# Kernel optimization log

Measured on AMD Instinct MI355X. Metric: run time of the kernel, lower is better.

## Reference

```python
import jax, jax.numpy as jnp
import numpy as np

HEADS = 20
NUM_AOE = 16
NUM_IP = 16


def setup_inputs() -> dict:
    key = jax.random.key(0)
    ks = jax.random.split(key, 7)
    B, Sq, H = 8, 4096, 1280
    Skv, C = 109, 768
    scale = 0.02
    return {
        "hidden_states": jax.random.normal(ks[0], (B, Sq, H), jnp.float32),
        "encoder_hidden_states": jax.random.normal(ks[1], (B, Skv, C), jnp.float32),
        "Wq": jax.random.normal(ks[2], (H, H), jnp.float32) * scale,
        "Wk": jax.random.normal(ks[3], (C, H), jnp.float32) * scale,
        "Wv": jax.random.normal(ks[4], (C, H), jnp.float32) * scale,
        "Wo": jax.random.normal(ks[5], (H, H), jnp.float32) * scale,
        "bo": jnp.zeros((H,), jnp.float32),
    }


def reference(hidden_states, encoder_hidden_states, Wq, Wk, Wv, Wo, bo):
    B, Sq, H = hidden_states.shape
    Skv = encoder_hidden_states.shape[1]
    head_dim = H // HEADS
    residual = hidden_states

    # projections (no bias on q/k/v, as in diffusers SD attention)
    q = (hidden_states @ Wq).reshape(B, Sq, HEADS, head_dim).transpose(0, 2, 1, 3)
    k = (encoder_hidden_states @ Wk).reshape(B, Skv, HEADS, head_dim).transpose(0, 2, 1, 3)
    v = (encoder_hidden_states @ Wv).reshape(B, Skv, HEADS, head_dim).transpose(0, 2, 1, 3)

    # manual attention: QK^T / sqrt(d), softmax
    scores = jnp.einsum("bhqd,bhkd->bhqk", q, k) / jnp.sqrt(jnp.asarray(head_dim, q.dtype))
    probs = jax.nn.softmax(scores, axis=-1)

    # frequency_mode != 'both': rescale aoe (first NUM_AOE) and image (last NUM_IP)
    # key-token ranges post-softmax, then renormalize. scale_aoe = scale_ip = 1
    # in this config, but the renormalization math is kept faithfully.
    scale_aoe = jnp.asarray(1.0, probs.dtype)
    scale_ip = jnp.asarray(1.0, probs.dtype)
    idx = jnp.arange(Skv)
    scale_vector = jnp.where(idx < NUM_AOE, scale_aoe, 1.0)
    scale_vector = jnp.where(idx >= Skv - NUM_IP, scale_vector * scale_ip, scale_vector)
    probs = probs * scale_vector  # broadcasts over (B, HEADS, Sq, Skv)
    probs = probs / probs.sum(axis=-1, keepdims=True)

    out = jnp.einsum("bhqk,bhkd->bhqd", probs, v)
    out = out.transpose(0, 2, 1, 3).reshape(B, Sq, H)
    out = out @ Wo + bo
    # residual connection, rescale_output_factor = 1.0
    return out + residual
```

## Files before the change

kernel.cpp:

```cpp
#include <hip/hip_runtime.h>
#include <hip/hip_bf16.h>

typedef unsigned short u16;
typedef __attribute__((ext_vector_type(8))) short short8;
typedef __attribute__((ext_vector_type(4))) short short4v;
typedef __attribute__((ext_vector_type(4))) float f32x4;

#define HEADS 20
#define HD 64
#define BB 8
#define SQ 4096
#define HDIM 1280
#define SKV 109
#define CDIM 768
#define SKV_PAD 128
#define SKV_T 112

#define SBAR() asm volatile("s_barrier" ::: "memory")

static __device__ __forceinline__ u16 f2bf(float x) {
  union { __hip_bfloat16 h; u16 u; } cv;
  cv.h = __float2bfloat16(x);
  return cv.u;
}

static __device__ __forceinline__ void gll16(const void* g, void* l) {
  __builtin_amdgcn_global_load_lds(
      (const __attribute__((address_space(1))) unsigned int*)g,
      (__attribute__((address_space(3))) unsigned int*)l, 16, 0, 0);
}

__global__ __launch_bounds__(256) void tcvt(const float* __restrict__ W,
                                            u16* __restrict__ out, int K, int N,
                                            float scale) {
  __shared__ float t[32][33];
  int tx = threadIdx.x & 31, ty = threadIdx.x >> 5;
  int n0 = blockIdx.x * 32, k0 = blockIdx.y * 32;
#pragma unroll
  for (int i = 0; i < 32; i += 8)
    t[ty + i][tx] = W[(size_t)(k0 + ty + i) * N + n0 + tx];
  __syncthreads();
#pragma unroll
  for (int i = 0; i < 32; i += 8)
    out[(size_t)(n0 + ty + i) * K + k0 + tx] = f2bf(t[tx][ty + i] * scale);
}

__global__ __launch_bounds__(256) void ehs_prep(const float* __restrict__ e,
                                                u16* __restrict__ out) {
  int idx = blockIdx.x * 256 + threadIdx.x;
  if (idx >= BB * SKV_PAD * CDIM / 4) return;
  int c4 = idx * 4;
  int b = c4 / (SKV_PAD * CDIM);
  int rem = c4 - b * (SKV_PAD * CDIM);
  int s = rem / CDIM;
  int c = rem - s * CDIM;
  short4v o = {0, 0, 0, 0};
  if (s < SKV) {
    f32x4 v = *(const f32x4*)(e + ((size_t)b * SKV + s) * CDIM + c);
#pragma unroll
    for (int j = 0; j < 4; j++) o[j] = (short)f2bf(v[j]);
  }
  *(short4v*)&out[c4] = o;
}

__global__ __launch_bounds__(256) void hscvt(const float* __restrict__ in,
                                             u16* __restrict__ out) {
  const size_t total = (size_t)BB * SQ * HDIM;
  size_t step = (size_t)gridDim.x * 256 * 8;
  for (size_t i = ((size_t)blockIdx.x * 256 + threadIdx.x) * 8; i < total;
       i += step) {
    f32x4 a = *(const f32x4*)(in + i);
    f32x4 b = *(const f32x4*)(in + i + 4);
    short8 o;
#pragma unroll
    for (int j = 0; j < 4; j++) {
      o[j] = (short)f2bf(a[j]);
      o[j + 4] = (short)f2bf(b[j]);
    }
    *(short8*)&out[i] = o;
  }
}


static __device__ __forceinline__ void stage_half(u16* region,
                                                  const u16* gbase, int K,
                                                  int tid) {
#pragma unroll
  for (int j = 0; j < 2; ++j) {
    int c = tid + j * 512;
    int s = c ^ ((c >> 3) & 7);
    gll16(gbase + (size_t)(s >> 3) * K + (s & 7) * 8, region + c * 8);
  }
}

static __device__ __forceinline__ short8 lread(const u16* region, int row,
                                               int kcol) {
  int idx = (row * 64 + kcol) ^ ((row & 7) << 3);
  return *(const short8*)(region + idx);
}

template <int MODE>
__global__ __launch_bounds__(512, 2)
void gemm256(const u16* __restrict__ A, const u16* __restrict__ Bt,
             void* __restrict__ outp, int K, int ntn,
             const float* __restrict__ bias, const float* __restrict__ resid) {
  __shared__ u16 lds[2][2][2][8192];
  const int tid = threadIdx.x;
  const int wid = tid >> 6, lane = tid & 63;
  const int wm = wid >> 2, wn = wid & 3;
  const int g = lane >> 4, r = lane & 15;

  const int nwg = gridDim.x;
  const int orig = blockIdx.x;
  const int wg = (orig & 7) * (nwg >> 3) + (orig >> 3);
  const int mt = wg / ntn, nt = wg - mt * ntn;
  const int row0 = mt * 256, col0 = nt * 256;

  const u16* Ag = A + (size_t)row0 * K;
  const u16* Bg = Bt + (size_t)col0 * K;
  const int NT = K >> 6;

  f32x4 acc[8][4] = {};

  stage_half(&lds[0][0][0][0], Ag, K, tid);
  stage_half(&lds[0][0][1][0], Ag + (size_t)128 * K, K, tid);
  stage_half(&lds[0][1][0][0], Bg, K, tid);
  stage_half(&lds[0][1][1][0], Bg + (size_t)128 * K, K, tid);
  stage_half(&lds[1][1][0][0], Bg + 64, K, tid);
  stage_half(&lds[1][1][1][0], Bg + (size_t)128 * K + 64, K, tid);
  asm volatile("s_waitcnt vmcnt(4)" ::: "memory");
  SBAR();

  for (int t = 0; t < NT; ++t) {
    const int cur = t & 1, nxt = cur ^ 1;
    const u16* Ac = &lds[cur][0][wm][0];
    const u16* Bc = &lds[cur][1][wn >> 1][0];
    const int brow = (wn & 1) * 64;
    short8 a0[4][2], a1[4][2], b0[2][2], b1[2][2];

#pragma unroll
    for (int mi = 0; mi < 4; ++mi)
#pragma unroll
      for (int ks = 0; ks < 2; ++ks)
        a0[mi][ks] = lread(Ac, mi * 16 + r, ks * 32 + g * 8);
#pragma unroll
    for (int nf = 0; nf < 2; ++nf)
#pragma unroll
      for (int ks = 0; ks < 2; ++ks)
        b0[nf][ks] = lread(Bc, brow + nf * 16 + r, ks * 32 + g * 8);
    if (t + 1 < NT)
      stage_half(&lds[nxt][0][0][0], Ag + (size_t)(t + 1) * 64, K, tid);
    SBAR();
    __builtin_amdgcn_s_setprio(1);
#pragma unroll
    for (int mi = 0; mi < 4; ++mi)
#pragma unroll
      for (int nf = 0; nf < 2; ++nf)
#pragma unroll
        for (int ks = 0; ks < 2; ++ks)
          acc[mi][nf] = __builtin_amdgcn_mfma_f32_16x16x32_bf16(
              a0[mi][ks], b0[nf][ks], acc[mi][nf], 0, 0, 0);
    __builtin_amdgcn_s_setprio(0);
    SBAR();

#pragma unroll
    for (int nf = 0; nf < 2; ++nf)
#pragma unroll
      for (int ks = 0; ks < 2; ++ks)
        b1[nf][ks] = lread(Bc, brow + 32 + nf * 16 + r, ks * 32 + g * 8);
    if (t + 1 < NT)
      stage_half(&lds[nxt][0][1][0], Ag + (size_t)128 * K + (size_t)(t + 1) * 64,
                 K, tid);
    SBAR();
    __builtin_amdgcn_s_setprio(1);
#pragma unroll
    for (int mi = 0; mi < 4; ++mi)
#pragma unroll
      for (int nf = 0; nf < 2; ++nf)
#pragma unroll
        for (int ks = 0; ks < 2; ++ks)
          acc[mi][2 + nf] = __builtin_amdgcn_mfma_f32_16x16x32_bf16(
              a0[mi][ks], b1[nf][ks], acc[mi][2 + nf], 0, 0, 0);
    __builtin_amdgcn_s_setprio(0);
    SBAR();

#pragma unroll
    for (int mi = 0; mi < 4; ++mi)
#pragma unroll
      for (int ks = 0; ks < 2; ++ks)
        a1[mi][ks] = lread(Ac, 64 + mi * 16 + r, ks * 32 + g * 8);
    if (t + 2 < NT)
      stage_half(&lds[cur][1][0][0], Bg + (size_t)(t + 2) * 64, K, tid);
    SBAR();
    __builtin_amdgcn_s_setprio(1);
#pragma unroll
    for (int mi = 0; mi < 4; ++mi)
#pragma unroll
      for (int nf = 0; nf < 2; ++nf)
#pragma unroll
        for (int ks = 0; ks < 2; ++ks)
          acc[4 + mi][2 + nf] = __builtin_amdgcn_mfma_f32_16x16x32_bf16(
              a1[mi][ks], b1[nf][ks], acc[4 + mi][2 + nf], 0, 0, 0);
    __builtin_amdgcn_s_setprio(0);
    SBAR();

    if (t + 2 < NT)
      stage_half(&lds[cur][1][1][0], Bg + (size_t)128 * K + (size_t)(t + 2) * 64,
                 K, tid);
    if (t < NT - 2)
      asm volatile("s_waitcnt vmcnt(4)" ::: "memory");
    else
      asm volatile("s_waitcnt vmcnt(0)" ::: "memory");
    SBAR();
    __builtin_amdgcn_s_setprio(1);
#pragma unroll
    for (int mi = 0; mi < 4; ++mi)
#pragma unroll
      for (int nf = 0; nf < 2; ++nf)
#pragma unroll
        for (int ks = 0; ks < 2; ++ks)
          acc[4 + mi][nf] = __builtin_amdgcn_mfma_f32_16x16x32_bf16(
              a1[mi][ks], b0[nf][ks], acc[4 + mi][nf], 0, 0, 0);
    __builtin_amdgcn_s_setprio(0);
    SBAR();
  }

  if constexpr (MODE == 0) {
    u16* O = (u16*)outp;
#pragma unroll
    for (int am = 0; am < 8; ++am)
#pragma unroll
      for (int i = 0; i < 4; ++i) {
        size_t m = row0 + wm * 128 + am * 16 + g * 4 + i;
        size_t base = m * HDIM + col0 + wn * 64 + r;
#pragma unroll
        for (int an = 0; an < 4; ++an)
          O[base + an * 16] = f2bf(acc[am][an][i]);
      }
  } else {
    float* O = (float*)outp;
#pragma unroll
    for (int am = 0; am < 8; ++am)
#pragma unroll
      for (int i = 0; i < 4; ++i) {
        size_t m = row0 + wm * 128 + am * 16 + g * 4 + i;
        size_t base = m * HDIM + col0 + wn * 64 + r;
#pragma unroll
        for (int an = 0; an < 4; ++an) {
          int col = col0 + wn * 64 + an * 16 + r;
          O[base + an * 16] = acc[am][an][i] + bias[col] + resid[base + an * 16];
        }
      }
  }
}

template <int MODE>
__global__ __launch_bounds__(256, 4)
void gemm_glds(const u16* __restrict__ A, const u16* __restrict__ Bt,
               void* __restrict__ outp, int K, int ntn) {
  __shared__ u16 Alds[128 * 32];
  __shared__ u16 Blds[128 * 32];
  const int tid = threadIdx.x;
  const int wid = tid >> 6, lane = tid & 63;
  const int wm = wid >> 1, wn = wid & 1;
  const int g = lane >> 4, r = lane & 15;

  const int nwg = gridDim.x;
  const int orig = blockIdx.x;
  const int wg = (orig & 7) * (nwg >> 3) + (orig >> 3);
  const int mt = wg / ntn, nt = wg - mt * ntn;
  const int row0 = mt * 128, col0 = nt * 128;
  const int erow = tid >> 2, ecol = (tid & 3) * 8;

  f32x4 acc[4][4] = {};

  for (int kt = 0; kt < K; kt += 32) {
    const u16* ag = A + (size_t)(row0 + erow) * K + kt + ecol;
    const u16* bg = Bt + (size_t)(col0 + erow) * K + kt + ecol;
    gll16(ag, &Alds[erow * 32 + ecol]);
    gll16(ag + (size_t)64 * K, &Alds[(erow + 64) * 32 + ecol]);
    gll16(bg, &Blds[erow * 32 + ecol]);
    gll16(bg + (size_t)64 * K, &Blds[(erow + 64) * 32 + ecol]);
    __syncthreads();

    short8 afr[4], bfr[4];
#pragma unroll
    for (int mi = 0; mi < 4; mi++)
      afr[mi] = *(short8*)&Alds[(wm * 64 + mi * 16 + r) * 32 + g * 8];
#pragma unroll
    for (int ni = 0; ni < 4; ni++)
      bfr[ni] = *(short8*)&Blds[(wn * 64 + ni * 16 + r) * 32 + g * 8];
#pragma unroll
    for (int mi = 0; mi < 4; mi++)
#pragma unroll
      for (int ni = 0; ni < 4; ni++)
        acc[mi][ni] = __builtin_amdgcn_mfma_f32_16x16x32_bf16(afr[mi], bfr[ni],
                                                              acc[mi][ni], 0, 0, 0);
    __syncthreads();
  }

  u16* O = (u16*)outp;
#pragma unroll
  for (int mi = 0; mi < 4; mi++)
#pragma unroll
    for (int i = 0; i < 4; i++) {
      int m = row0 + wm * 64 + mi * 16 + g * 4 + i;
      int b = m >> 7, skv = m & 127;
#pragma unroll
      for (int ni = 0; ni < 4; ni++) {
        int col = col0 + wn * 64 + ni * 16 + r;
        int hh = col >> 6, d = col & 63;
        size_t addr;
        if constexpr (MODE == 1)
          addr = (((size_t)b * HEADS + hh) * SKV_PAD + skv) * HD + d;
        else
          addr = (((size_t)b * HEADS + hh) * HD + d) * SKV_PAD + skv;
        O[addr] = f2bf(acc[mi][ni][i]);
      }
    }
}

__global__ __launch_bounds__(256, 2)
void attn_kernel(const u16* __restrict__ q, const u16* __restrict__ kh,
                 const u16* __restrict__ vt, u16* __restrict__ o) {
  __shared__ u16 Klds[SKV_T * 72];
  __shared__ u16 Vlds[HD * 136];
  __shared__ u16 Plds[4 * 16 * 136];
  const int tid = threadIdx.x;
  const int wid = tid >> 6, lane = tid & 63;
  const int g = lane >> 4, r = lane & 15;
  const int qt = blockIdx.x;
  const int bh = blockIdx.y;
  const int b = bh / HEADS, h = bh - b * HEADS;

  const u16* kg = kh + (size_t)bh * SKV_PAD * HD;
  for (int i = tid; i < SKV_T * 8; i += 256) {
    int row = i >> 3, c = (i & 7) * 8;
    *(short8*)&Klds[row * 72 + c] = *(const short8*)(kg + row * HD + c);
  }
  const u16* vg = vt + (size_t)bh * HD * SKV_PAD;
  for (int i = tid; i < HD * 16; i += 256) {
    int row = i >> 4, c = (i & 15) * 8;
    *(short8*)&Vlds[row * 136 + c] = *(const short8*)(vg + row * SKV_PAD + c);
  }
  __syncthreads();

  const u16* qg = q + ((size_t)b * SQ + qt * 64 + wid * 16 + r) * HDIM + h * HD + g * 8;
  short8 aq0 = *(const short8*)(qg);
  short8 aq1 = *(const short8*)(qg + 32);

  f32x4 s[7];
#pragma unroll
  for (int nf = 0; nf < 7; nf++) {
    f32x4 z = {0.f, 0.f, 0.f, 0.f};
    short8 k0 = *(short8*)&Klds[(nf * 16 + r) * 72 + g * 8];
    short8 k1 = *(short8*)&Klds[(nf * 16 + r) * 72 + 32 + g * 8];
    z = __builtin_amdgcn_mfma_f32_16x16x32_bf16(aq0, k0, z, 0, 0, 0);
    z = __builtin_amdgcn_mfma_f32_16x16x32_bf16(aq1, k1, z, 0, 0, 0);
    s[nf] = z;
  }

  {
    short4v z = {0, 0, 0, 0};
    *(short4v*)&Plds[(wid * 16 + r) * 136 + 112 + g * 4] = z;
  }

#pragma unroll
  for (int i = 0; i < 4; i++) {
    float pv[7];
    float mx = -1e30f;
#pragma unroll
    for (int nf = 0; nf < 7; nf++) {
      float v = s[nf][i];
      if (nf == 6 && r >= 13) v = -1e30f;
      pv[nf] = v;
      mx = fmaxf(mx, v);
    }
#pragma unroll
    for (int d = 1; d < 16; d <<= 1) mx = fmaxf(mx, __shfl_xor(mx, d, 64));
    float sum = 0.f;
#pragma unroll
    for (int nf = 0; nf < 7; nf++) {
      float e = (nf == 6 && r >= 13) ? 0.f : __expf(pv[nf] - mx);
      pv[nf] = e;
      sum += e;
    }
#pragma unroll
    for (int d = 1; d < 16; d <<= 1) sum += __shfl_xor(sum, d, 64);
    float is = 1.f / sum;
#pragma unroll
    for (int nf = 0; nf < 7; nf++)
      Plds[(wid * 16 + g * 4 + i) * 136 + nf * 16 + r] = f2bf(pv[nf] * is);
  }
  __syncthreads();

  f32x4 oacc[4] = {};
#pragma unroll
  for (int kk = 0; kk < 4; kk++) {
    short8 ap = *(short8*)&Plds[(wid * 16 + r) * 136 + kk * 32 + g * 8];
#pragma unroll
    for (int nf = 0; nf < 4; nf++) {
      short8 bv = *(short8*)&Vlds[(nf * 16 + r) * 136 + kk * 32 + g * 8];
      oacc[nf] = __builtin_amdgcn_mfma_f32_16x16x32_bf16(ap, bv, oacc[nf], 0, 0, 0);
    }
  }
  u16* og = o + ((size_t)b * SQ + qt * 64 + wid * 16) * HDIM + h * HD;
#pragma unroll
  for (int nf = 0; nf < 4; nf++)
#pragma unroll
    for (int i = 0; i < 4; i++)
      og[(size_t)(g * 4 + i) * HDIM + nf * 16 + r] = f2bf(oacc[nf][i]);
}

extern "C" void kernel_launch(void* const* d_in, const int* in_sizes, int n_in,
                              void* d_out, int out_size, void* d_ws, size_t ws_size,
                              hipStream_t stream) {
  const float* hs  = (const float*)d_in[0];
  const float* ehs = (const float*)d_in[1];
  const float* Wq  = (const float*)d_in[2];
  const float* Wk  = (const float*)d_in[3];
  const float* Wv  = (const float*)d_in[4];
  const float* Wo  = (const float*)d_in[5];
  const float* bo  = (const float*)d_in[6];

  char* ws = (char*)d_ws;
  size_t off = 0;
  auto alloc = [&](size_t elems) {
    u16* p = (u16*)(ws + off);
    off += ((elems * 2 + 255) / 256) * 256;
    return p;
  };
  u16* wqt  = alloc((size_t)HDIM * HDIM);
  u16* wot  = alloc((size_t)HDIM * HDIM);
  u16* wkt  = alloc((size_t)HDIM * CDIM);
  u16* wvt  = alloc((size_t)HDIM * CDIM);
  u16* ehsp = alloc((size_t)BB * SKV_PAD * CDIM);
  u16* khb  = alloc((size_t)BB * HEADS * SKV_PAD * HD);
  u16* vtb  = alloc((size_t)BB * HEADS * HD * SKV_PAD);
  u16* qb   = alloc((size_t)BB * SQ * HDIM);
  u16* ao   = alloc((size_t)BB * SQ * HDIM);
  u16* hsb  = ao;

  tcvt<<<dim3(HDIM / 32, HDIM / 32), 256, 0, stream>>>(Wq, wqt, HDIM, HDIM, 0.125f);
  tcvt<<<dim3(HDIM / 32, CDIM / 32), 256, 0, stream>>>(Wk, wkt, CDIM, HDIM, 1.0f);
  tcvt<<<dim3(HDIM / 32, CDIM / 32), 256, 0, stream>>>(Wv, wvt, CDIM, HDIM, 1.0f);
  tcvt<<<dim3(HDIM / 32, HDIM / 32), 256, 0, stream>>>(Wo, wot, HDIM, HDIM, 1.0f);
  ehs_prep<<<dim3((BB * SKV_PAD * CDIM / 4 + 255) / 256), 256, 0, stream>>>(ehs, ehsp);
  hscvt<<<dim3(2048), 256, 0, stream>>>(hs, hsb);

  gemm_glds<1><<<dim3(80), 256, 0, stream>>>(ehsp, wkt, khb, CDIM, 10);
  gemm_glds<2><<<dim3(80), 256, 0, stream>>>(ehsp, wvt, vtb, CDIM, 10);
  gemm256<0><<<dim3(640), 512, 0, stream>>>(hsb, wqt, qb, HDIM, 5, nullptr, nullptr);
  attn_kernel<<<dim3(SQ / 64, BB * HEADS), 256, 0, stream>>>(qb, khb, vtb, ao);
  gemm256<3><<<dim3(640), 512, 0, stream>>>(ao, wot, (void*)d_out, HDIM, 5, bo, hs);
}
```

Measured before the change: 464.1 us.

## Reorder GEMM LDS staging so A tiles prefetch two steps ahead

Restructures the global-to-LDS prefetch schedule in the 256x256 bf16 GEMM. Both A halves are now staged two iterations ahead, and only one B half stays one iteration ahead. All A fragments (a0 and a1) are loaded from LDS at the start of each iteration, and the swizzle column offsets are precomputed once outside the loop. The waitcnt depth rises from 4 to 6 to keep more loads in flight. This hides more global latency and frees the later phases to issue only MFMAs, at the cost of more registers live at once and a tighter buffer-reuse ordering that must still be race-free.

Measured after the change: 487.5 us. 1.05x slower.

```diff
diff --git a/kernel.cpp b/kernel.cpp
--- a/kernel.cpp
+++ b/kernel.cpp
@@ -93,12 +93,6 @@
   }
 }
 
-static __device__ __forceinline__ short8 lread(const u16* region, int row,
-                                               int kcol) {
-  int idx = (row * 64 + kcol) ^ ((row & 7) << 3);
-  return *(const short8*)(region + idx);
-}
-
 template <int MODE>
 __global__ __launch_bounds__(512, 2)
 void gemm256(const u16* __restrict__ A, const u16* __restrict__ Bt,
@@ -119,6 +113,9 @@
   const u16* Ag = A + (size_t)row0 * K;
   const u16* Bg = Bt + (size_t)col0 * K;
   const int NT = K >> 6;
+  const int brow = (wn & 1) * 64;
+  const int cx0 = (g * 8) ^ ((r & 7) << 3);
+  const int cx1 = (32 + g * 8) ^ ((r & 7) << 3);
 
   f32x4 acc[8][4] = {};
 
@@ -126,30 +123,33 @@
   stage_half(&lds[0][0][1][0], Ag + (size_t)128 * K, K, tid);
   stage_half(&lds[0][1][0][0], Bg, K, tid);
   stage_half(&lds[0][1][1][0], Bg + (size_t)128 * K, K, tid);
+  stage_half(&lds[1][0][0][0], Ag + 64, K, tid);
+  stage_half(&lds[1][0][1][0], Ag + (size_t)128 * K + 64, K, tid);
   stage_half(&lds[1][1][0][0], Bg + 64, K, tid);
-  stage_half(&lds[1][1][1][0], Bg + (size_t)128 * K + 64, K, tid);
-  asm volatile("s_waitcnt vmcnt(4)" ::: "memory");
+  asm volatile("s_waitcnt vmcnt(6)" ::: "memory");
   SBAR();
 
   for (int t = 0; t < NT; ++t) {
     const int cur = t & 1, nxt = cur ^ 1;
     const u16* Ac = &lds[cur][0][wm][0];
     const u16* Bc = &lds[cur][1][wn >> 1][0];
-    const int brow = (wn & 1) * 64;
     short8 a0[4][2], a1[4][2], b0[2][2], b1[2][2];
 
 #pragma unroll
-    for (int mi = 0; mi < 4; ++mi)
-#pragma unroll
-      for (int ks = 0; ks < 2; ++ks)
-        a0[mi][ks] = lread(Ac, mi * 16 + r, ks * 32 + g * 8);
-#pragma unroll
-    for (int nf = 0; nf < 2; ++nf)
-#pragma unroll
-      for (int ks = 0; ks < 2; ++ks)
-        b0[nf][ks] = lread(Bc, brow + nf * 16 + r, ks * 32 + g * 8);
+    for (int mi = 0; mi < 4; ++mi) {
+      a0[mi][0] = *(const short8*)&Ac[(mi * 16 + r) * 64 + cx0];
+      a0[mi][1] = *(const short8*)&Ac[(mi * 16 + r) * 64 + cx1];
+      a1[mi][0] = *(const short8*)&Ac[(64 + mi * 16 + r) * 64 + cx0];
+      a1[mi][1] = *(const short8*)&Ac[(64 + mi * 16 + r) * 64 + cx1];
+    }
+#pragma unroll
+    for (int nf = 0; nf < 2; ++nf) {
+      b0[nf][0] = *(const short8*)&Bc[(brow + nf * 16 + r) * 64 + cx0];
+      b0[nf][1] = *(const short8*)&Bc[(brow + nf * 16 + r) * 64 + cx1];
+    }
     if (t + 1 < NT)
-      stage_half(&lds[nxt][0][0][0], Ag + (size_t)(t + 1) * 64, K, tid);
+      stage_half(&lds[nxt][1][1][0], Bg + (size_t)128 * K + (size_t)(t + 1) * 64,
+                 K, tid);
     SBAR();
     __builtin_amdgcn_s_setprio(1);
 #pragma unroll
@@ -164,13 +164,12 @@
     SBAR();
 
 #pragma unroll
-    for (int nf = 0; nf < 2; ++nf)
-#pragma unroll
-      for (int ks = 0; ks < 2; ++ks)
-        b1[nf][ks] = lread(Bc, brow + 32 + nf * 16 + r, ks * 32 + g * 8);
-    if (t + 1 < NT)
-      stage_half(&lds[nxt][0][1][0], Ag + (size_t)128 * K + (size_t)(t + 1) * 64,
-                 K, tid);
+    for (int nf = 0; nf < 2; ++nf) {
+      b1[nf][0] = *(const short8*)&Bc[(brow + 32 + nf * 16 + r) * 64 + cx0];
+      b1[nf][1] = *(const short8*)&Bc[(brow + 32 + nf * 16 + r) * 64 + cx1];
+    }
+    if (t + 2 < NT)
+      stage_half(&lds[cur][0][0][0], Ag + (size_t)(t + 2) * 64, K, tid);
     SBAR();
     __builtin_amdgcn_s_setprio(1);
 #pragma unroll
@@ -184,13 +183,9 @@
     __builtin_amdgcn_s_setprio(0);
     SBAR();
 
-#pragma unroll
-    for (int mi = 0; mi < 4; ++mi)
-#pragma unroll
-      for (int ks = 0; ks < 2; ++ks)
-        a1[mi][ks] = lread(Ac, 64 + mi * 16 + r, ks * 32 + g * 8);
     if (t + 2 < NT)
-      stage_half(&lds[cur][1][0][0], Bg + (size_t)(t + 2) * 64, K, tid);
+      stage_half(&lds[cur][0][1][0], Ag + (size_t)128 * K + (size_t)(t + 2) * 64,
+                 K, tid);
     SBAR();
     __builtin_amdgcn_s_setprio(1);
 #pragma unroll
@@ -205,10 +200,9 @@
     SBAR();
 
     if (t + 2 < NT)
-      stage_half(&lds[cur][1][1][0], Bg + (size_t)128 * K + (size_t)(t + 2) * 64,
-                 K, tid);
+      stage_half(&lds[cur][1][0][0], Bg + (size_t)(t + 2) * 64, K, tid);
     if (t < NT - 2)
-      asm volatile("s_waitcnt vmcnt(4)" ::: "memory");
+      asm volatile("s_waitcnt vmcnt(6)" ::: "memory");
     else
       asm volatile("s_waitcnt vmcnt(0)" ::: "memory");
     SBAR();
```
